# Kernel optimization log

Measured on AMD Instinct MI355X. Metric: run time of the kernel, lower is better.

The kernel has to match this reference:

```python
import jax, jax.numpy as jnp
import numpy as np

NEG_BIG = 10000000000.0  # matches tf source's -1e10 mask fill


def setup_inputs() -> dict:
    key = jax.random.key(0)
    k1, k2, k3 = jax.random.split(key, 3)
    B, H, T, D = 2, 12, 4096, 64
    return {
        "q": jax.random.normal(k1, (B, H, T, D), dtype=jnp.float32),
        "k": jax.random.normal(k2, (B, H, T, D), dtype=jnp.float32),
        "v": jax.random.normal(k3, (B, H, T, D), dtype=jnp.float32),
        "localAttention": 256,
    }


def _band_mask(nd, ns, local_attention, dtype):
    # 1's in the lower triangle counting from the lower-right corner,
    # optionally restricted to a local window of width `local_attention`.
    i = jnp.arange(nd)[:, None]
    j = jnp.arange(ns)[None, :]
    m = i >= j - ns + nd
    if local_attention > 0:
        m = m & (i < j - ns + nd + local_attention)
    return m.astype(dtype)


def reference(q, k, v, localAttention):
    # q,k,v: [B, H, T, D]
    dimv = v.shape[-1]
    w = jnp.einsum("bhqd,bhkd->bhqk", q, k) * (1.0 / np.sqrt(dimv))
    nd, ns = w.shape[2], w.shape[3]
    b = _band_mask(nd, ns, localAttention, w.dtype)[None, None]  # [1,1,nd,ns]
    w = w * b - jnp.asarray(NEG_BIG, w.dtype) * (1 - b)
    sm = jax.nn.softmax(w, axis=-1)
    out = jnp.einsum("bhqk,bhkd->bhqd", sm, v)       # [B,H,T,Dv]
    out = jnp.transpose(out, (0, 2, 1, 3))            # [B,T,H,Dv]
    B, T, H, Dv = out.shape
    return out.reshape(B, T, H * Dv)
```

## Files before the change

### kernel.cpp

```cpp
#include <hip/hip_runtime.h>

#define TT 4096
#define DD 64
#define HH 12
#define NTILE 10

typedef __attribute__((ext_vector_type(8))) short s8v;
typedef __attribute__((ext_vector_type(4))) short s4v;
typedef __attribute__((ext_vector_type(4))) float f4v;

static __device__ __forceinline__ short f2bf(float f) {
  unsigned u = __builtin_bit_cast(unsigned, f);
  u += 0x7FFFu + ((u >> 16) & 1u);
  return (short)(u >> 16);
}

static __device__ __forceinline__ s8v pack8(float4 a, float4 b) {
  s8v r;
  r[0] = f2bf(a.x); r[1] = f2bf(a.y); r[2] = f2bf(a.z); r[3] = f2bf(a.w);
  r[4] = f2bf(b.x); r[5] = f2bf(b.y); r[6] = f2bf(b.z); r[7] = f2bf(b.w);
  return r;
}

static __device__ __forceinline__ f4v MFMA16(s4v a, s4v b, f4v c) {
#if defined(__has_builtin) && __has_builtin(__builtin_amdgcn_mfma_f32_16x16x16bf16_1k)
  return __builtin_amdgcn_mfma_f32_16x16x16bf16_1k(a, b, c, 0, 0, 0);
#else
  asm volatile("v_mfma_f32_16x16x16_bf16 %0, %1, %2, %0\n\ts_nop 7\n\ts_nop 7"
               : "+v"(c) : "v"(a), "v"(b));
  return c;
#endif
}

__global__ __launch_bounds__(256, 4)
void lma_attn_kernel(const float* __restrict__ Q, const float* __restrict__ K,
                     const float* __restrict__ V, const int* __restrict__ laPtr,
                     float* __restrict__ out)
{
  __shared__ short k_lds[32 * 64];
  __shared__ short vt_lds[64 * 32];
  __shared__ float o_lds[64][65];

  const int tid = threadIdx.x;
  const int bid = blockIdx.x;
  const int qt = bid & 63;
  const int bh = bid >> 6;
  const int q0 = qt << 6;
  const int la = laPtr[0];

  const int lane = tid & 63;
  const int w = tid >> 6;
  const int c = lane & 15;
  const int g = lane >> 4;
  const int qw0 = q0 + w * 16;
  const int i_row = qw0 + c;
  int jlo = i_row - la + 1; if (jlo < 0) jlo = 0;

  const size_t base = (size_t)bh * (TT * DD);

  s8v qf[2];
  {
    const float* qp = Q + base + (size_t)i_row * DD + 8 * g;
    float4 a0 = *(const float4*)(qp);
    float4 a1 = *(const float4*)(qp + 4);
    float4 b0 = *(const float4*)(qp + 32);
    float4 b1 = *(const float4*)(qp + 36);
    qf[0] = pack8(a0, a1);
    qf[1] = pack8(b0, b1);
  }

  f4v acc_o[4] = {{0.f,0.f,0.f,0.f},{0.f,0.f,0.f,0.f},
                  {0.f,0.f,0.f,0.f},{0.f,0.f,0.f,0.f}};
  float m = -1e30f;
  float lsum = 0.f;

  const int jr = tid >> 3;
  const int d0 = (tid & 7) * 8;

  for (int t = 0; t < NTILE; ++t) {
    const int kj0 = q0 - 256 + 32 * t;
    if (kj0 < 0) continue;

    __syncthreads();
    {
      const float* kp = K + base + (size_t)(kj0 + jr) * DD + d0;
      float4 ka = *(const float4*)kp;
      float4 kb = *(const float4*)(kp + 4);
      const int slot = (tid & 7) ^ (jr & 7);
      *(s8v*)&k_lds[jr * 64 + slot * 8] = pack8(ka, kb);

      const float* vp = V + base + (size_t)(kj0 + jr) * DD + d0;
      float4 va = *(const float4*)vp;
      float4 vb = *(const float4*)(vp + 4);
      float vv[8] = {va.x, va.y, va.z, va.w, vb.x, vb.y, vb.z, vb.w};
      #pragma unroll
      for (int e = 0; e < 8; ++e) {
        const int d = d0 + e;
        const int sv = (jr >> 3) ^ ((d >> 1) & 3);
        vt_lds[d * 32 + sv * 8 + (jr & 7)] = f2bf(vv[e]);
      }
    }
    __syncthreads();

    const bool active = (kj0 <= qw0 + 15) && (kj0 + 31 >= qw0 - la + 1);
    if (active) {
      f4v sacc[2] = {{0.f,0.f,0.f,0.f},{0.f,0.f,0.f,0.f}};
      #pragma unroll
      for (int ch = 0; ch < 2; ++ch) {
        const int slot = ((ch << 2) + g) ^ (c & 7);
        s8v kf0 = *(const s8v*)&k_lds[(c) * 64 + slot * 8];
        s8v kf1 = *(const s8v*)&k_lds[(16 + c) * 64 + slot * 8];
        sacc[0] = __builtin_amdgcn_mfma_f32_16x16x32_bf16(kf0, qf[ch], sacc[0], 0, 0, 0);
        sacc[1] = __builtin_amdgcn_mfma_f32_16x16x32_bf16(kf1, qf[ch], sacc[1], 0, 0, 0);
      }

      float p[2][4];
      float tmax = -1e30f;
      #pragma unroll
      for (int sub = 0; sub < 2; ++sub)
        #pragma unroll
        for (int r = 0; r < 4; ++r) {
          const int jt = kj0 + 16 * sub + 4 * g + r;
          float s = sacc[sub][r] * 0.125f;
          s = (jt >= jlo && jt <= i_row) ? s : -1e30f;
          p[sub][r] = s;
          tmax = fmaxf(tmax, s);
        }
      tmax = fmaxf(tmax, __shfl_xor(tmax, 16, 64));
      tmax = fmaxf(tmax, __shfl_xor(tmax, 32, 64));
      const float mnew = fmaxf(m, tmax);
      const float corr = __expf(m - mnew);
      m = mnew;

      float psum = 0.f;
      s4v pb[2];
      #pragma unroll
      for (int sub = 0; sub < 2; ++sub)
        #pragma unroll
        for (int r = 0; r < 4; ++r) {
          const float e = __expf(p[sub][r] - mnew);
          psum += e;
          pb[sub][r] = f2bf(e);
        }
      psum += __shfl_xor(psum, 16, 64);
      psum += __shfl_xor(psum, 32, 64);
      lsum = lsum * corr + psum;
      #pragma unroll
      for (int dt = 0; dt < 4; ++dt) {
        acc_o[dt][0] *= corr; acc_o[dt][1] *= corr;
        acc_o[dt][2] *= corr; acc_o[dt][3] *= corr;
      }

      #pragma unroll
      for (int dt = 0; dt < 4; ++dt) {
        const int d = dt * 16 + c;
        #pragma unroll
        for (int sub = 0; sub < 2; ++sub) {
          const int sv = ((sub << 1) + (g >> 1)) ^ ((c >> 1) & 3);
          s4v vf = *(const s4v*)&vt_lds[d * 32 + sv * 8 + 4 * (g & 1)];
          acc_o[dt] = MFMA16(vf, pb[sub], acc_o[dt]);
        }
      }
    }
  }

  const float inv = 1.f / lsum;
  #pragma unroll
  for (int dt = 0; dt < 4; ++dt)
    #pragma unroll
    for (int r = 0; r < 4; ++r)
      o_lds[w * 16 + c][dt * 16 + 4 * g + r] = acc_o[dt][r] * inv;
  __syncthreads();
  {
    const int row = tid >> 2;
    const int col0 = (tid & 3) << 4;
    const int b = bh / HH;
    const int h = bh % HH;
    float* op = out + ((size_t)b * TT + (q0 + row)) * (HH * DD) + h * DD + col0;
    #pragma unroll
    for (int x = 0; x < 4; ++x)
      *(float4*)(op + 4 * x) = *(const float4*)&o_lds[row][col0 + 4 * x];
  }
}

extern "C" void kernel_launch(void* const* d_in, const int* in_sizes, int n_in,
                              void* d_out, int out_size, void* d_ws, size_t ws_size,
                              hipStream_t stream) {
  const float* q = (const float*)d_in[0];
  const float* k = (const float*)d_in[1];
  const float* v = (const float*)d_in[2];
  const int* la = (const int*)d_in[3];
  float* out = (float*)d_out;
  (void)in_sizes; (void)n_in; (void)out_size; (void)d_ws; (void)ws_size;

  dim3 grid(24 * 64);
  dim3 block(256);
  lma_attn_kernel<<<grid, block, 0, stream>>>(q, k, v, la, out);
}
```

Baseline: 139.7 us.

## Double-buffer 64-key tiles with 128-query blocks and register prefetch

Each workgroup now handles 128 queries (two 16-row groups per wave) and 64-key tiles, with double-buffered LDS and register prefetch of the next K/V tile while the current one is computed. This halves the number of syncs per key and overlaps global loads with MFMA work. It also swizzles block IDs across XCDs, switches to exp2 with a folded log2e scale, uses a padded V-transpose layout, and stores output directly instead of through LDS. The window bound is now hardcoded to 256 (LAMAX) for the tile count, the grid is halved, and register pressure rises (launch bounds 3).

```diff
diff --git a/kernel.cpp b/kernel.cpp
--- a/kernel.cpp
+++ b/kernel.cpp
@@ -3,10 +3,14 @@
 #define TT 4096
 #define DD 64
 #define HH 12
-#define NTILE 10
+#define LAMAX 256
+#define KT 64
+#define NT 6
+#define VS 68
 
 typedef __attribute__((ext_vector_type(8))) short s8v;
 typedef __attribute__((ext_vector_type(4))) short s4v;
+typedef __attribute__((ext_vector_type(2))) short s2v;
 typedef __attribute__((ext_vector_type(4))) float f4v;
 
 static __device__ __forceinline__ short f2bf(float f) {
@@ -32,154 +36,162 @@
 #endif
 }
 
-__global__ __launch_bounds__(256, 4)
+__global__ __launch_bounds__(256, 3)
 void lma_attn_kernel(const float* __restrict__ Q, const float* __restrict__ K,
                      const float* __restrict__ V, const int* __restrict__ laPtr,
                      float* __restrict__ out)
 {
-  __shared__ short k_lds[32 * 64];
-  __shared__ short vt_lds[64 * 32];
-  __shared__ float o_lds[64][65];
-
-  const int tid = threadIdx.x;
+  __shared__ short k_lds[2][64 * 64];
+  __shared__ short vt_lds[2][64 * VS];
+
+  const int tid  = threadIdx.x;
+  const int lane = tid & 63;
+  const int w    = tid >> 6;
+  const int c    = lane & 15;
+  const int g    = lane >> 4;
+
   const int bid = blockIdx.x;
-  const int qt = bid & 63;
-  const int bh = bid >> 6;
-  const int q0 = qt << 6;
-  const int la = laPtr[0];
-
-  const int lane = tid & 63;
-  const int w = tid >> 6;
-  const int c = lane & 15;
-  const int g = lane >> 4;
-  const int qw0 = q0 + w * 16;
-  const int i_row = qw0 + c;
-  int jlo = i_row - la + 1; if (jlo < 0) jlo = 0;
+  const int wg  = (bid & 7) * 96 + (bid >> 3);
+  const int bh  = wg >> 5;
+  const int q0  = (wg & 31) << 7;
+  const int la  = laPtr[0];
 
   const size_t base = (size_t)bh * (TT * DD);
-
-  s8v qf[2];
-  {
-    const float* qp = Q + base + (size_t)i_row * DD + 8 * g;
-    float4 a0 = *(const float4*)(qp);
-    float4 a1 = *(const float4*)(qp + 4);
-    float4 b0 = *(const float4*)(qp + 32);
-    float4 b1 = *(const float4*)(qp + 36);
-    qf[0] = pack8(a0, a1);
-    qf[1] = pack8(b0, b1);
+  const int qw0 = q0 + w * 32;
+
+  s8v qf[2][2];
+  #pragma unroll
+  for (int rg = 0; rg < 2; ++rg) {
+    const float* qp = Q + base + (size_t)(qw0 + rg * 16 + c) * DD + 8 * g;
+    qf[rg][0] = pack8(*(const float4*)qp,        *(const float4*)(qp + 4));
+    qf[rg][1] = pack8(*(const float4*)(qp + 32), *(const float4*)(qp + 36));
   }
 
-  f4v acc_o[4] = {{0.f,0.f,0.f,0.f},{0.f,0.f,0.f,0.f},
-                  {0.f,0.f,0.f,0.f},{0.f,0.f,0.f,0.f}};
-  float m = -1e30f;
-  float lsum = 0.f;
-
-  const int jr = tid >> 3;
-  const int d0 = (tid & 7) * 8;
-
-  for (int t = 0; t < NTILE; ++t) {
-    const int kj0 = q0 - 256 + 32 * t;
-    if (kj0 < 0) continue;
-
-    __syncthreads();
-    {
-      const float* kp = K + base + (size_t)(kj0 + jr) * DD + d0;
-      float4 ka = *(const float4*)kp;
-      float4 kb = *(const float4*)(kp + 4);
-      const int slot = (tid & 7) ^ (jr & 7);
-      *(s8v*)&k_lds[jr * 64 + slot * 8] = pack8(ka, kb);
-
-      const float* vp = V + base + (size_t)(kj0 + jr) * DD + d0;
-      float4 va = *(const float4*)vp;
-      float4 vb = *(const float4*)(vp + 4);
-      float vv[8] = {va.x, va.y, va.z, va.w, vb.x, vb.y, vb.z, vb.w};
-      #pragma unroll
-      for (int e = 0; e < 8; ++e) {
-        const int d = d0 + e;
-        const int sv = (jr >> 3) ^ ((d >> 1) & 3);
-        vt_lds[d * 32 + sv * 8 + (jr & 7)] = f2bf(vv[e]);
+  const int kj  = tid >> 2;
+  const int kd0 = (tid & 3) << 4;
+  const int vj0 = (tid & 31) << 1;
+  const int vd0 = (tid >> 5) << 3;
+
+  float4 kr0, kr1, kr2, kr3, vr0, vr1, vr2, vr3;
+  auto stage_load = [&](int kj0) {
+    const float* kp = K + base + (size_t)(kj0 + kj) * DD + kd0;
+    kr0 = *(const float4*)kp;        kr1 = *(const float4*)(kp + 4);
+    kr2 = *(const float4*)(kp + 8);  kr3 = *(const float4*)(kp + 12);
+    const float* vp = V + base + (size_t)(kj0 + vj0) * DD + vd0;
+    vr0 = *(const float4*)vp;        vr1 = *(const float4*)(vp + 4);
+    vr2 = *(const float4*)(vp + DD); vr3 = *(const float4*)(vp + DD + 4);
+  };
+  auto stage_write = [&](int buf) {
+    short* kb = (short*)k_lds[buf];
+    const int sw = kj & 7, g8 = kd0 >> 3;
+    *(s8v*)&kb[kj * 64 + ((g8    ) ^ sw) * 8] = pack8(kr0, kr1);
+    *(s8v*)&kb[kj * 64 + ((g8 + 1) ^ sw) * 8] = pack8(kr2, kr3);
+    short* vb = (short*)vt_lds[buf];
+    const float a0[8] = {vr0.x, vr0.y, vr0.z, vr0.w, vr1.x, vr1.y, vr1.z, vr1.w};
+    const float a1[8] = {vr2.x, vr2.y, vr2.z, vr2.w, vr3.x, vr3.y, vr3.z, vr3.w};
+    #pragma unroll
+    for (int e = 0; e < 8; ++e) {
+      s2v pr; pr[0] = f2bf(a0[e]); pr[1] = f2bf(a1[e]);
+      *(s2v*)&vb[(vd0 + e) * VS + vj0] = pr;
+    }
+  };
+
+  f4v acc[2][4] = {};
+  float m2[2]   = {-1e30f, -1e30f};
+  float lsum[2] = {0.f, 0.f};
+  const float SCL = 0.125f * 1.44269504f;
+
+  const int t0 = (q0 >= LAMAX) ? 0 : ((LAMAX - q0) >> 6);
+
+  stage_load(q0 - LAMAX + (t0 << 6));
+  stage_write(t0 & 1);
+  __syncthreads();
+
+  for (int t = t0; t < NT; ++t) {
+    const int cb  = t & 1;
+    const int kj0 = q0 - LAMAX + (t << 6);
+    if (t + 1 < NT) stage_load(kj0 + KT);
+
+    const short* kb = (const short*)k_lds[cb];
+    const short* vb = (const short*)vt_lds[cb];
+
+    #pragma unroll
+    for (int rg = 0; rg < 2; ++rg) {
+      const int rb = qw0 + (rg << 4);
+      if (!((kj0 <= rb + 15) && (kj0 + KT >= rb - la + 2))) continue;
+      const int i_row = rb + c;
+      const int jlo = i_row - la + 1;
+
+      f4v sa[4] = {};
+      #pragma unroll
+      for (int ch = 0; ch < 2; ++ch) {
+        #pragma unroll
+        for (int ks = 0; ks < 4; ++ks) {
+          s8v kf = *(const s8v*)&kb[(ks * 16 + c) * 64 + (((ch << 2) + g) ^ (c & 7)) * 8];
+          sa[ks] = __builtin_amdgcn_mfma_f32_16x16x32_bf16(kf, qf[rg][ch], sa[ks], 0, 0, 0);
+        }
+      }
+
+      float p[4][4]; float tmax = -1e30f;
+      #pragma unroll
+      for (int ks = 0; ks < 4; ++ks)
+        #pragma unroll
+        for (int r = 0; r < 4; ++r) {
+          const int jt = kj0 + ks * 16 + 4 * g + r;
+          float s = sa[ks][r] * SCL;
+          s = (jt >= jlo && jt <= i_row) ? s : -1e30f;
+          p[ks][r] = s; tmax = fmaxf(tmax, s);
+        }
+      tmax = fmaxf(tmax, __shfl_xor(tmax, 16, 64));
+      tmax = fmaxf(tmax, __shfl_xor(tmax, 32, 64));
+      const float mn = fmaxf(m2[rg], tmax);
+      const float corr = exp2f(m2[rg] - mn);
+      m2[rg] = mn;
+
+      s4v pb[4]; float ps = 0.f;
+      #pragma unroll
+      for (int ks = 0; ks < 4; ++ks)
+        #pragma unroll
+        for (int r = 0; r < 4; ++r) {
+          const float e = exp2f(p[ks][r] - mn);
+          ps += e; pb[ks][r] = f2bf(e);
+        }
+      ps += __shfl_xor(ps, 16, 64);
+      ps += __shfl_xor(ps, 32, 64);
+      lsum[rg] = lsum[rg] * corr + ps;
+      #pragma unroll
+      for (int dt = 0; dt < 4; ++dt) {
+        acc[rg][dt][0] *= corr; acc[rg][dt][1] *= corr;
+        acc[rg][dt][2] *= corr; acc[rg][dt][3] *= corr;
+      }
+
+      #pragma unroll
+      for (int dt = 0; dt < 4; ++dt) {
+        const int d = dt * 16 + c;
+        #pragma unroll
+        for (int sub = 0; sub < 4; ++sub) {
+          s4v vf = *(const s4v*)&vb[d * VS + sub * 16 + g * 4];
+          acc[rg][dt] = MFMA16(vf, pb[sub], acc[rg][dt]);
+        }
       }
     }
+
+    if (t + 1 < NT) stage_write((t + 1) & 1);
     __syncthreads();
-
-    const bool active = (kj0 <= qw0 + 15) && (kj0 + 31 >= qw0 - la + 1);
-    if (active) {
-      f4v sacc[2] = {{0.f,0.f,0.f,0.f},{0.f,0.f,0.f,0.f}};
-      #pragma unroll
-      for (int ch = 0; ch < 2; ++ch) {
-        const int slot = ((ch << 2) + g) ^ (c & 7);
-        s8v kf0 = *(const s8v*)&k_lds[(c) * 64 + slot * 8];
-        s8v kf1 = *(const s8v*)&k_lds[(16 + c) * 64 + slot * 8];
-        sacc[0] = __builtin_amdgcn_mfma_f32_16x16x32_bf16(kf0, qf[ch], sacc[0], 0, 0, 0);
-        sacc[1] = __builtin_amdgcn_mfma_f32_16x16x32_bf16(kf1, qf[ch], sacc[1], 0, 0, 0);
-      }
-
-      float p[2][4];
-      float tmax = -1e30f;
-      #pragma unroll
-      for (int sub = 0; sub < 2; ++sub)
-        #pragma unroll
-        for (int r = 0; r < 4; ++r) {
-          const int jt = kj0 + 16 * sub + 4 * g + r;
-          float s = sacc[sub][r] * 0.125f;
-          s = (jt >= jlo && jt <= i_row) ? s : -1e30f;
-          p[sub][r] = s;
-          tmax = fmaxf(tmax, s);
-        }
-      tmax = fmaxf(tmax, __shfl_xor(tmax, 16, 64));
-      tmax = fmaxf(tmax, __shfl_xor(tmax, 32, 64));
-      const float mnew = fmaxf(m, tmax);
-      const float corr = __expf(m - mnew);
-      m = mnew;
-
-      float psum = 0.f;
-      s4v pb[2];
-      #pragma unroll
-      for (int sub = 0; sub < 2; ++sub)
-        #pragma unroll
-        for (int r = 0; r < 4; ++r) {
-          const float e = __expf(p[sub][r] - mnew);
-          psum += e;
-          pb[sub][r] = f2bf(e);
-        }
-      psum += __shfl_xor(psum, 16, 64);
-      psum += __shfl_xor(psum, 32, 64);
-      lsum = lsum * corr + psum;
-      #pragma unroll
-      for (int dt = 0; dt < 4; ++dt) {
-        acc_o[dt][0] *= corr; acc_o[dt][1] *= corr;
-        acc_o[dt][2] *= corr; acc_o[dt][3] *= corr;
-      }
-
-      #pragma unroll
-      for (int dt = 0; dt < 4; ++dt) {
-        const int d = dt * 16 + c;
-        #pragma unroll
-        for (int sub = 0; sub < 2; ++sub) {
-          const int sv = ((sub << 1) + (g >> 1)) ^ ((c >> 1) & 3);
-          s4v vf = *(const s4v*)&vt_lds[d * 32 + sv * 8 + 4 * (g & 1)];
-          acc_o[dt] = MFMA16(vf, pb[sub], acc_o[dt]);
-        }
-      }
+  }
+
+  #pragma unroll
+  for (int rg = 0; rg < 2; ++rg) {
+    const float inv = 1.f / lsum[rg];
+    const int row = qw0 + (rg << 4) + c;
+    float* op = out + ((size_t)(bh / HH) * TT + row) * (HH * DD) + (bh % HH) * DD + 4 * g;
+    #pragma unroll
+    for (int dt = 0; dt < 4; ++dt) {
+      float4 o;
+      o.x = acc[rg][dt][0] * inv; o.y = acc[rg][dt][1] * inv;
+      o.z = acc[rg][dt][2] * inv; o.w = acc[rg][dt][3] * inv;
+      *(float4*)(op + dt * 16) = o;
     }
-  }
-
-  const float inv = 1.f / lsum;
-  #pragma unroll
-  for (int dt = 0; dt < 4; ++dt)
-    #pragma unroll
-    for (int r = 0; r < 4; ++r)
-      o_lds[w * 16 + c][dt * 16 + 4 * g + r] = acc_o[dt][r] * inv;
-  __syncthreads();
-  {
-    const int row = tid >> 2;
-    const int col0 = (tid & 3) << 4;
-    const int b = bh / HH;
-    const int h = bh % HH;
-    float* op = out + ((size_t)b * TT + (q0 + row)) * (HH * DD) + h * DD + col0;
-    #pragma unroll
-    for (int x = 0; x < 4; ++x)
-      *(float4*)(op + 4 * x) = *(const float4*)&o_lds[row][col0 + 4 * x];
   }
 }
 
@@ -193,7 +205,7 @@
   float* out = (float*)d_out;
   (void)in_sizes; (void)n_in; (void)out_size; (void)d_ws; (void)ws_size;
 
-  dim3 grid(24 * 64);
+  dim3 grid(24 * 32);
   dim3 block(256);
   lma_attn_kernel<<<grid, block, 0, stream>>>(q, k, v, la, out);
 }
```

Result: no change. 141.1 us (+1.0%).
